# Performance work log

Measured on AMD Instinct MI355X. Metric: run time of the kernel, lower is better.

## Reference

```python
import jax, jax.numpy as jnp
import numpy as np

H = 1024
V = 32000
L = 15
B = 512


def setup_inputs() -> dict:
    key = jax.random.key(0)
    ks = jax.random.split(key, 16)
    s = 0.02
    return {
        "input_ids": jax.random.randint(ks[0], (B,), 0, V),
        "hidden": jax.random.normal(ks[1], (1, B, H), jnp.float32),
        "encoder_outputs": jax.random.normal(ks[2], (L, B, H), jnp.float32),
        "max_length": L,
        "embedding": jax.random.normal(ks[3], (V, H), jnp.float32) * s,
        "attn1_w": jax.random.normal(ks[4], (1, 2 * H), jnp.float32) * s,
        "attn1_b": jnp.zeros((1,), jnp.float32),
        "combine_w": jax.random.normal(ks[5], (H, 2 * H), jnp.float32) * s,
        "combine_b": jnp.zeros((H,), jnp.float32),
        "w_ih": jax.random.normal(ks[6], (3 * H, H), jnp.float32) * s,
        "w_hh": jax.random.normal(ks[7], (3 * H, H), jnp.float32) * s,
        "b_ih": jnp.zeros((3 * H,), jnp.float32),
        "b_hh": jnp.zeros((3 * H,), jnp.float32),
        "out_w": jax.random.normal(ks[8], (V, H), jnp.float32) * s,
        "out_b": jnp.zeros((V,), jnp.float32),
    }


def reference(input_ids, hidden, encoder_outputs, max_length, embedding,
              attn1_w, attn1_b, combine_w, combine_b,
              w_ih, w_hh, b_ih, b_hh, out_w, out_b):
    # embedding lookup (dropout is identity in eval mode)
    emb = embedding[input_ids]                       # [B, H]
    # Bahdanau-style additive scores: vectorize the per-step python loop
    emb_l = jnp.broadcast_to(emb[None], (max_length, B, H))   # [L, B, H]
    cat = jnp.concatenate([emb_l, encoder_outputs], axis=-1)  # [L, B, 2H]
    scores = cat @ attn1_w.T + attn1_b               # [L, B, 1]
    attn_weights = jax.nn.softmax(scores, axis=0)    # softmax over L
    ctx = jnp.sum(attn_weights * encoder_outputs, axis=0)     # [B, H]
    x = jnp.concatenate([emb, ctx], axis=-1) @ combine_w.T + combine_b  # [B, H]
    # n_layers = 1: relu then one GRU step (seq len 1)
    x = jax.nn.relu(x)
    h = hidden[0]                                    # [B, H]
    gi = x @ w_ih.T + b_ih                           # [B, 3H]
    gh = h @ w_hh.T + b_hh                           # [B, 3H]
    i_r, i_z, i_n = jnp.split(gi, 3, axis=1)
    h_r, h_z, h_n = jnp.split(gh, 3, axis=1)
    r = jax.nn.sigmoid(i_r + h_r)
    z = jax.nn.sigmoid(i_z + h_z)
    n = jnp.tanh(i_n + r * h_n)
    h_new = (1.0 - z) * n + z * h                    # [B, H]
    logits = h_new @ out_w.T + out_b                 # [B, V]
    output = jax.nn.log_softmax(logits, axis=1)
    return output, h_new[None], attn_weights
```

## Files before the change

### kernel.cpp

```cpp
#include <hip/hip_runtime.h>

#define HH 1024
#define VV 32000
#define LL 15
#define BB 512

typedef __bf16 bf16;
typedef __bf16 bf16x4 __attribute__((ext_vector_type(4)));
typedef __bf16 bf16x8 __attribute__((ext_vector_type(8)));
typedef float f32x4 __attribute__((ext_vector_type(4)));

#define VMCNT(n) asm volatile("s_waitcnt vmcnt(" #n ")" ::: "memory")
#define SBAR     __builtin_amdgcn_s_barrier()
#define SCHED0   __builtin_amdgcn_sched_barrier(0)

__device__ __forceinline__ unsigned short f2bf(float f) {
    unsigned int u = __float_as_uint(f);
    unsigned int r = (u + 0x7fffu + ((u >> 16) & 1u)) >> 16;
    return (unsigned short)r;
}

__device__ __forceinline__ void gld_lds16(const void* g, void* l) {
    __builtin_amdgcn_global_load_lds(
        (const __attribute__((address_space(1))) unsigned int*)g,
        (__attribute__((address_space(3))) unsigned int*)l, 16, 0, 0);
}

__global__ __launch_bounds__(256)
void cvt4_kernel(const float* __restrict__ a0, unsigned short* __restrict__ o0, int n0_,
                 const float* __restrict__ a1, unsigned short* __restrict__ o1, int n1_,
                 const float* __restrict__ a2, unsigned short* __restrict__ o2, int n2_,
                 const float* __restrict__ a3, unsigned short* __restrict__ o3, int n3_) {
    int i = blockIdx.x * 256 + threadIdx.x;
    const float* src; unsigned short* dst;
    if (i < n0_) { src = a0; dst = o0; }
    else if ((i -= n0_) < n1_) { src = a1; dst = o1; }
    else if ((i -= n1_) < n2_) { src = a2; dst = o2; }
    else if ((i -= n2_) < n3_) { src = a3; dst = o3; }
    else return;
    const f32x4 a = ((const f32x4*)src)[2 * i], b = ((const f32x4*)src)[2 * i + 1];
    ((bf16x4*)dst)[2 * i]     = __builtin_convertvector(a, bf16x4);
    ((bf16x4*)dst)[2 * i + 1] = __builtin_convertvector(b, bf16x4);
}

__global__ __launch_bounds__(256)
void pack_w(const float* __restrict__ src, unsigned short* __restrict__ dst) {
    const int b = blockIdx.x;
    const int g = b >> 2, q = b & 3;
    const float* pan = src + (size_t)g * 65536;
    char* pd = (char*)(dst + (size_t)g * 65536);
    #pragma unroll
    for (int j = 0; j < 16; j++) {
        const int s4 = q * 4096 + j * 256 + threadIdx.x;
        const f32x4 v = ((const f32x4*)pan)[s4];
        const int sp = s4 * 4;
        const int r = sp >> 10, k = sp & 1023;
        bf16x4 w = __builtin_convertvector(v, bf16x4);
        *(bf16x4*)(pd + ((k >> 6) << 13) + (r << 7) + ((k & 63) << 1)) = w;
    }
}

__global__ __launch_bounds__(256)
void attn_kernel(const int* __restrict__ ids, const float* __restrict__ enc,
                 const float* __restrict__ embedding,
                 const float* __restrict__ attn1_w, const float* __restrict__ attn1_b,
                 float* __restrict__ attn_out, unsigned short* __restrict__ cat_out) {
    const int b = blockIdx.x, tid = threadIdx.x;
    const int lane = tid & 63, wv = tid >> 6;

    __shared__ float s_enc[LL * HH];
    __shared__ float s_scores[LL];
    __shared__ float s_red[4];

    for (int idx = tid; idx < LL * HH / 4; idx += 256) {
        const int l = (idx * 4) >> 10, h = (idx * 4) & (HH - 1);
        *(f32x4*)&s_enc[idx * 4] = *(const f32x4*)&enc[((size_t)l * BB + b) * HH + h];
    }

    const float* embr = embedding + (size_t)ids[b] * HH;
    float p = 0.f;
    for (int j = tid; j < HH; j += 256) p += embr[j] * attn1_w[j];
    #pragma unroll
    for (int o = 32; o; o >>= 1) p += __shfl_xor(p, o);
    if (lane == 0) s_red[wv] = p;
    __syncthreads();
    const float semb = s_red[0] + s_red[1] + s_red[2] + s_red[3] + attn1_b[0];

    for (int l = wv; l < LL; l += 4) {
        float q = 0.f;
        for (int j = lane; j < HH; j += 64) q += s_enc[l * HH + j] * attn1_w[HH + j];
        #pragma unroll
        for (int o = 32; o; o >>= 1) q += __shfl_xor(q, o);
        if (lane == 0) s_scores[l] = q + semb;
    }
    __syncthreads();

    float mx = -3.4e38f;
    #pragma unroll
    for (int l = 0; l < LL; l++) mx = fmaxf(mx, s_scores[l]);
    float aw[LL], sum = 0.f;
    #pragma unroll
    for (int l = 0; l < LL; l++) { aw[l] = __expf(s_scores[l] - mx); sum += aw[l]; }
    const float inv = 1.f / sum;
    #pragma unroll
    for (int l = 0; l < LL; l++) aw[l] *= inv;

    if (tid < LL) attn_out[tid * BB + b] = aw[tid];

    for (int j = tid; j < HH; j += 256) {
        float c = 0.f;
        #pragma unroll
        for (int l = 0; l < LL; l++) c += aw[l] * s_enc[l * HH + j];
        cat_out[(size_t)b * (2 * HH) + j] = f2bf(embr[j]);
        cat_out[(size_t)b * (2 * HH) + HH + j] = f2bf(c);
    }
}

template<int TM, int TN, int OUT, int GATES>
__global__ __launch_bounds__(256)
void gemm_nt(const bf16* __restrict__ A, const bf16* __restrict__ B,
             const float* __restrict__ bias, void* __restrict__ Cout,
             const bf16* __restrict__ A2, const bf16* __restrict__ B2,
             const float* __restrict__ bias2, void* __restrict__ C2,
             const int K, const int N) {
    constexpr int FM = TM / 32, FN = TN / 32;
    __shared__ bf16 As[2][TM * 64];
    __shared__ bf16 Bs[2][TN * 64];

    if (GATES && blockIdx.z == 1) { A = A2; B = B2; bias = bias2; Cout = C2; }

    const int tid = threadIdx.x;
    const int lane = tid & 63, wave = tid >> 6;
    const int wm = wave >> 1, wn = wave & 1;
    const int rlo = lane & 15, khi = lane >> 4;
    const int m0 = blockIdx.y * TM, n0 = blockIdx.x * TN;

    f32x4 acc[FM][FN] = {};
    constexpr int IA = TM / 32, IB = TN / 32;

    auto stage = [&](int k0, int buf) {
        #pragma unroll
        for (int i = 0; i < IA; i++) {
            const int p = (i * 256 + tid) * 16;
            const int row = p >> 7;
            const int qs = (p & 127) ^ ((row & 7) << 4);
            gld_lds16(A + (size_t)(m0 + row) * K + k0 + (qs >> 1),
                      &As[buf][0] + i * 2048 + wave * 512);
        }
        #pragma unroll
        for (int i = 0; i < IB; i++) {
            const int p = (i * 256 + tid) * 16;
            const int row = p >> 7;
            const int qs = (p & 127) ^ ((row & 7) << 4);
            gld_lds16(B + (size_t)(n0 + row) * K + k0 + (qs >> 1),
                      &Bs[buf][0] + i * 2048 + wave * 512);
        }
    };

    auto compute = [&](int buf) {
        #pragma unroll
        for (int ks = 0; ks < 2; ks++) {
            bf16x8 af[FM], bfr[FN];
            #pragma unroll
            for (int m = 0; m < FM; m++) {
                const int r = wm * (TM / 2) + m * 16 + rlo;
                const int sw = (ks * 64 + khi * 16) ^ ((r & 7) << 4);
                af[m] = *(const bf16x8*)((const char*)&As[buf][0] + r * 128 + sw);
            }
            #pragma unroll
            for (int n = 0; n < FN; n++) {
                const int r = wn * (TN / 2) + n * 16 + rlo;
                const int sw = (ks * 64 + khi * 16) ^ ((r & 7) << 4);
                bfr[n] = *(const bf16x8*)((const char*)&Bs[buf][0] + r * 128 + sw);
            }
            #pragma unroll
            for (int m = 0; m < FM; m++)
                #pragma unroll
                for (int n = 0; n < FN; n++)
                    acc[m][n] = __builtin_amdgcn_mfma_f32_16x16x32_bf16(af[m], bfr[n], acc[m][n], 0, 0, 0);
        }
    };

    const int NT = K >> 6;
    stage(0, 0);
    stage(64, 1);

    for (int kt = 0; kt < NT; kt += 2) {
        {
            const int t = kt;
            if (t + 1 < NT) { VMCNT(4); } else { VMCNT(0); }
            SCHED0; SBAR; SCHED0;
            compute(0);
            SCHED0; SBAR; SCHED0;
            if (t + 2 < NT) stage((t + 2) << 6, 0);
        }
        {
            const int t = kt + 1;
            if (t + 1 < NT) { VMCNT(4); } else { VMCNT(0); }
            SCHED0; SBAR; SCHED0;
            compute(1);
            SCHED0; SBAR; SCHED0;
            if (t + 2 < NT) stage((t + 2) << 6, 1);
        }
    }

    #pragma unroll
    for (int m = 0; m < FM; m++) {
        const int gr = m0 + wm * (TM / 2) + m * 16 + khi * 4;
        #pragma unroll
        for (int n = 0; n < FN; n++) {
            const int gc = n0 + wn * (TN / 2) + n * 16 + rlo;
            const float bv = bias[gc];
            #pragma unroll
            for (int j = 0; j < 4; j++) {
                float v = acc[m][n][j] + bv;
                if (OUT == 1) {
                    v = fmaxf(v, 0.f);
                    ((unsigned short*)Cout)[(size_t)(gr + j) * N + gc] = f2bf(v);
                } else {
                    ((float*)Cout)[(size_t)(gr + j) * N + gc] = v;
                }
            }
        }
    }
}

__global__ __launch_bounds__(256, 3)
void gemm_out(const bf16* __restrict__ A, const bf16* __restrict__ Bp,
              const float* __restrict__ bias, float* __restrict__ C,
              float* __restrict__ pmax, float* __restrict__ psum, const int nbase) {
    constexpr int K = HH, N = VV;
    __shared__ bf16 As[2][128 * 64];
    __shared__ bf16 Bs[2][64 * 64];
    __shared__ float sPm[2][128], sPs[2][128];

    const int tid = threadIdx.x;
    const int lane = tid & 63, wave = tid >> 6;
    const int wm = wave >> 1, wn = wave & 1;
    const int rlo = lane & 15, khi = lane >> 4;

    constexpr int gridN = 250;
    constexpr int nFull = (gridN >> 3) << 5;
    const int bidx = blockIdx.x;
    int g, jm;
    if (bidx < nFull) { const int s = bidx >> 5, rem = bidx & 31; jm = rem >> 3; g = s * 8 + (rem & 7); }
    else { const int rem = bidx - nFull; constexpr int gleft = gridN & 7; g = (gridN & ~7) + rem % gleft; jm = rem / gleft; }
    const int n0 = nbase + g * 64, m0 = jm * 128;

    const char* tile_base = (const char*)Bp + (size_t)g * 131072;

    f32x4 acc[4][2] = {};

    auto stage = [&](int k0, int buf) {
        #pragma unroll
        for (int i = 0; i < 4; i++) {
            const int p = (i * 256 + tid) * 16;
            const int row = p >> 7;
            const int qs = (p & 127) ^ ((row & 7) << 4);
            gld_lds16(A + (size_t)(m0 + row) * K + k0 + (qs >> 1),
                      &As[buf][0] + i * 2048 + wave * 512);
        }
        #pragma unroll
        for (int i = 0; i < 2; i++) {
            const int p = (i * 256 + tid) * 16;
            const int row = p >> 7;
            const int qs = (p & 127) ^ ((row & 7) << 4);
            gld_lds16(tile_base + (size_t)k0 * 128 + row * 128 + qs,
                      &Bs[buf][0] + i * 2048 + wave * 512);
        }
    };

    auto compute = [&](int buf) {
        #pragma unroll
        for (int ks = 0; ks < 2; ks++) {
            bf16x8 af[4], bfr[2];
            #pragma unroll
            for (int m = 0; m < 4; m++) {
                const int r = wm * 64 + m * 16 + rlo;
                const int sw = (ks * 64 + khi * 16) ^ ((r & 7) << 4);
                af[m] = *(const bf16x8*)((const char*)&As[buf][0] + r * 128 + sw);
            }
            #pragma unroll
            for (int n = 0; n < 2; n++) {
                const int r = wn * 32 + n * 16 + rlo;
                const int sw = (ks * 64 + khi * 16) ^ ((r & 7) << 4);
                bfr[n] = *(const bf16x8*)((const char*)&Bs[buf][0] + r * 128 + sw);
            }
            #pragma unroll
            for (int m = 0; m < 4; m++)
                #pragma unroll
                for (int n = 0; n < 2; n++)
                    acc[m][n] = __builtin_amdgcn_mfma_f32_16x16x32_bf16(af[m], bfr[n], acc[m][n], 0, 0, 0);
        }
    };

    constexpr int NT = K >> 6;
    stage(0, 0);
    stage(64, 1);

    for (int kt = 0; kt < NT; kt += 2) {
        {
            const int t = kt;
            if (t + 1 < NT) { VMCNT(6); } else { VMCNT(0); }
            SCHED0; SBAR; SCHED0;
            compute(0);
            SCHED0; SBAR; SCHED0;
            if (t + 2 < NT) stage((t + 2) << 6, 0);
        }
        {
            const int t = kt + 1;
            if (t + 1 < NT) { VMCNT(6); } else { VMCNT(0); }
            SCHED0; SBAR; SCHED0;
            compute(1);
            SCHED0; SBAR; SCHED0;
            if (t + 2 < NT) stage((t + 2) << 6, 1);
        }
    }

    float bvn[2];
    #pragma unroll
    for (int n = 0; n < 2; n++) bvn[n] = bias[n0 + wn * 32 + n * 16 + rlo];

    #pragma unroll
    for (int m = 0; m < 4; m++) {
        const int rbase = wm * 64 + m * 16 + khi * 4;
        #pragma unroll
        for (int j = 0; j < 4; j++) {
            const int gr = m0 + rbase + j;
            float v[2];
            #pragma unroll
            for (int n = 0; n < 2; n++) {
                v[n] = acc[m][n][j] + bvn[n];
                C[(size_t)gr * N + n0 + wn * 32 + n * 16 + rlo] = v[n];
            }
            float lm = fmaxf(v[0], v[1]);
            #pragma unroll
            for (int o = 8; o; o >>= 1) lm = fmaxf(lm, __shfl_xor(lm, o));
            float ls = __expf(v[0] - lm) + __expf(v[1] - lm);
            #pragma unroll
            for (int o = 8; o; o >>= 1) ls += __shfl_xor(ls, o);
            if (rlo == 0) { sPm[wn][rbase + j] = lm; sPs[wn][rbase + j] = ls; }
        }
    }
    __syncthreads();
    if (tid < 128) {
        const float ma = sPm[0][tid], mb = sPm[1][tid];
        const float M = fmaxf(ma, mb);
        const float S = sPs[0][tid] * __expf(ma - M) + sPs[1][tid] * __expf(mb - M);
        const int gg = (nbase >> 6) + g;
        pmax[(size_t)(m0 + tid) * 512 + gg] = M;
        psum[(size_t)(m0 + tid) * 512 + gg] = S;
    }
}

__global__ __launch_bounds__(256)
void gru_kernel(const float* __restrict__ gi, const float* __restrict__ gh,
                const float* __restrict__ h, float* __restrict__ hnew,
                unsigned short* __restrict__ hnew_bf) {
    const int i = blockIdx.x * 256 + threadIdx.x;
    const int e = i * 4;
    const int b = e >> 10, j = e & (HH - 1);
    const size_t o = ((size_t)b * 3 * HH + j) / 4;
    const f32x4 ir = ((const f32x4*)gi)[o],          iz = ((const f32x4*)gi)[o + HH / 4],
                in_ = ((const f32x4*)gi)[o + 2 * HH / 4];
    const f32x4 hr = ((const f32x4*)gh)[o],          hz = ((const f32x4*)gh)[o + HH / 4],
                hn = ((const f32x4*)gh)[o + 2 * HH / 4];
    const f32x4 hv = ((const f32x4*)h)[i];
    f32x4 out;
    ushort4 ob;
    #pragma unroll
    for (int c = 0; c < 4; c++) {
        const float r = 1.f / (1.f + __expf(-(ir[c] + hr[c])));
        const float z = 1.f / (1.f + __expf(-(iz[c] + hz[c])));
        const float n = tanhf(in_[c] + r * hn[c]);
        const float v = (1.f - z) * n + z * hv[c];
        out[c] = v;
        ((unsigned short*)&ob)[c] = f2bf(v);
    }
    ((f32x4*)hnew)[i] = out;
    ((ushort4*)hnew_bf)[i] = ob;
}

__global__ __launch_bounds__(512)
void lsm_final(const float* __restrict__ pmax, const float* __restrict__ psum,
               float* __restrict__ logits) {
    const int b = blockIdx.x, tid = threadIdx.x;
    const int lane = tid & 63, wv = tid >> 6;
    __shared__ float sm[8], ss[8];

    float m = -3.4e38f, s = 0.f;
    if (tid < VV / 64) { m = pmax[(size_t)b * 512 + tid]; s = psum[(size_t)b * 512 + tid]; }
    #pragma unroll
    for (int o = 32; o; o >>= 1) {
        const float mo = __shfl_xor(m, o), so = __shfl_xor(s, o);
        const float nm = fmaxf(m, mo);
        s = s * __expf(m - nm) + so * __expf(mo - nm);
        m = nm;
    }
    if (lane == 0) { sm[wv] = m; ss[wv] = s; }
    __syncthreads();
    float M = sm[0], S;
    #pragma unroll
    for (int w = 1; w < 8; w++) M = fmaxf(M, sm[w]);
    S = ss[0] * __expf(sm[0] - M);
    #pragma unroll
    for (int w = 1; w < 8; w++) S += ss[w] * __expf(sm[w] - M);
    const float lse = M + __logf(S);

    float* row = logits + (size_t)b * VV;
    for (int j = tid; j < VV / 4; j += 512) {
        f32x4 v = ((const f32x4*)row)[j];
        v[0] -= lse; v[1] -= lse; v[2] -= lse; v[3] -= lse;
        ((f32x4*)row)[j] = v;
    }
}

extern "C" void kernel_launch(void* const* d_in, const int* in_sizes, int n_in,
                              void* d_out, int out_size, void* d_ws, size_t ws_size,
                              hipStream_t stream) {
    const int*   ids       = (const int*)d_in[0];
    const float* hidden    = (const float*)d_in[1];
    const float* enc       = (const float*)d_in[2];
    const float* embedding = (const float*)d_in[4];
    const float* attn1_w   = (const float*)d_in[5];
    const float* attn1_b   = (const float*)d_in[6];
    const float* combine_w = (const float*)d_in[7];
    const float* combine_b = (const float*)d_in[8];
    const float* w_ih      = (const float*)d_in[9];
    const float* w_hh      = (const float*)d_in[10];
    const float* b_ih      = (const float*)d_in[11];
    const float* b_hh      = (const float*)d_in[12];
    const float* out_w     = (const float*)d_in[13];
    const float* out_b     = (const float*)d_in[14];

    float* out_lsm = (float*)d_out;
    float* out_h   = out_lsm + (size_t)BB * VV;
    float* out_aw  = out_h + (size_t)BB * HH;

    char* w = (char*)d_ws;
    unsigned short* w_ih_bf  = (unsigned short*)w;   w += (size_t)3 * HH * HH * 2;
    unsigned short* w_hh_bf  = (unsigned short*)w;   w += (size_t)3 * HH * HH * 2;
    unsigned short* w_cb_bf  = (unsigned short*)w;   w += (size_t)2 * HH * HH * 2;
    unsigned short* cat_bf   = (unsigned short*)w;   w += (size_t)BB * 2 * HH * 2;
    unsigned short* x_bf     = (unsigned short*)w;   w += (size_t)BB * HH * 2;
    unsigned short* hid_bf   = (unsigned short*)w;   w += (size_t)BB * HH * 2;
    unsigned short* hnew_bf  = (unsigned short*)w;   w += (size_t)BB * HH * 2;
    float* gi   = (float*)w;                         w += (size_t)BB * 3 * HH * 4;
    float* gh   = (float*)w;                         w += (size_t)BB * 3 * HH * 4;
    float* pmax = (float*)w;                         w += (size_t)BB * 512 * 4;
    float* psum = (float*)w;                         w += (size_t)BB * 512 * 4;
    unsigned short* packed = (unsigned short*)w;     w += (size_t)16000 * HH * 2;

    cvt4_kernel<<<(3 * HH * HH / 8 * 2 + 2 * HH * HH / 8 + BB * HH / 8) / 256, 256, 0, stream>>>(
        w_ih, w_ih_bf, 3 * HH * HH / 8,
        w_hh, w_hh_bf, 3 * HH * HH / 8,
        combine_w, w_cb_bf, 2 * HH * HH / 8,
        hidden, hid_bf, BB * HH / 8);

    attn_kernel<<<BB, 256, 0, stream>>>(ids, enc, embedding, attn1_w, attn1_b, out_aw, cat_bf);

    gemm_nt<64, 64, 1, 0><<<dim3(HH / 64, BB / 64), 256, 0, stream>>>(
        (const bf16*)cat_bf, (const bf16*)w_cb_bf, combine_b, x_bf,
        nullptr, nullptr, nullptr, nullptr, 2 * HH, HH);

    gemm_nt<64, 64, 0, 1><<<dim3(3 * HH / 64, BB / 64, 2), 256, 0, stream>>>(
        (const bf16*)hid_bf, (const bf16*)w_hh_bf, b_hh, gh,
        (const bf16*)x_bf, (const bf16*)w_ih_bf, b_ih, gi, HH, 3 * HH);

    gru_kernel<<<(BB * HH / 4) / 256, 256, 0, stream>>>(gi, gh, hidden, out_h, hnew_bf);

    pack_w<<<1000, 256, 0, stream>>>(out_w, packed);
    gemm_out<<<1000, 256, 0, stream>>>(
        (const bf16*)hnew_bf, (const bf16*)packed, out_b, out_lsm, pmax, psum, 0);

    pack_w<<<1000, 256, 0, stream>>>(out_w + (size_t)16000 * HH, packed);
    gemm_out<<<1000, 256, 0, stream>>>(
        (const bf16*)hnew_bf, (const bf16*)packed, out_b, out_lsm, pmax, psum, 16000);

    lsm_final<<<BB, 512, 0, stream>>>(pmax, psum, out_lsm);
}
```

Baseline: 208.6 us.

## Pack full output weight once and widen vocab GEMM tile to 128 columns

The output projection weight is now packed to bf16 in one pass into a full-size workspace buffer before the other kernels. This replaces two half-size pack/GEMM pairs with one GEMM launch. The GEMM tile grows from 128x64 to 128x128, so each wave holds a 4x4 MFMA accumulator block and A-tile reuse doubles. Occupancy is lowered from 3 to 2 blocks per CU, and the partial softmax buffers shrink to 250 column groups per row. The cost is more LDS and registers per block and a larger workspace.

```diff
diff --git a/kernel.cpp b/kernel.cpp
--- a/kernel.cpp
+++ b/kernel.cpp
@@ -24,6 +24,24 @@
     __builtin_amdgcn_global_load_lds(
         (const __attribute__((address_space(1))) unsigned int*)g,
         (__attribute__((address_space(3))) unsigned int*)l, 16, 0, 0);
+}
+
+__global__ __launch_bounds__(256)
+void pack_w(const float* __restrict__ src, unsigned short* __restrict__ dst) {
+    const int bid = blockIdx.x;
+    const int g = bid >> 3, rq = bid & 7;
+    const float* s0 = src + ((size_t)g * 128 + rq * 16) * 1024;
+    unsigned short* d0 = dst + (size_t)g * (16 * 128 * 64);
+    #pragma unroll
+    for (int j = 0; j < 16; j++) {
+        const int s4 = j * 256 + threadIdx.x;
+        const f32x4 v = ((const f32x4*)s0)[s4];
+        const int sp = s4 * 4;
+        const int rl = rq * 16 + (sp >> 10);
+        const int k = sp & 1023;
+        bf16x4 w = __builtin_convertvector(v, bf16x4);
+        *(bf16x4*)&d0[(size_t)(k >> 6) * 8192 + rl * 64 + (k & 63)] = w;
+    }
 }
 
 __global__ __launch_bounds__(256)
@@ -44,23 +62,6 @@
 }
 
 __global__ __launch_bounds__(256)
-void pack_w(const float* __restrict__ src, unsigned short* __restrict__ dst) {
-    const int b = blockIdx.x;
-    const int g = b >> 2, q = b & 3;
-    const float* pan = src + (size_t)g * 65536;
-    char* pd = (char*)(dst + (size_t)g * 65536);
-    #pragma unroll
-    for (int j = 0; j < 16; j++) {
-        const int s4 = q * 4096 + j * 256 + threadIdx.x;
-        const f32x4 v = ((const f32x4*)pan)[s4];
-        const int sp = s4 * 4;
-        const int r = sp >> 10, k = sp & 1023;
-        bf16x4 w = __builtin_convertvector(v, bf16x4);
-        *(bf16x4*)(pd + ((k >> 6) << 13) + (r << 7) + ((k & 63) << 1)) = w;
-    }
-}
-
-__global__ __launch_bounds__(256)
 void attn_kernel(const int* __restrict__ ids, const float* __restrict__ enc,
                  const float* __restrict__ embedding,
                  const float* __restrict__ attn1_w, const float* __restrict__ attn1_b,
@@ -225,13 +226,13 @@
     }
 }
 
-__global__ __launch_bounds__(256, 3)
+__global__ __launch_bounds__(256, 2)
 void gemm_out(const bf16* __restrict__ A, const bf16* __restrict__ Bp,
               const float* __restrict__ bias, float* __restrict__ C,
-              float* __restrict__ pmax, float* __restrict__ psum, const int nbase) {
+              float* __restrict__ pmax, float* __restrict__ psum) {
     constexpr int K = HH, N = VV;
     __shared__ bf16 As[2][128 * 64];
-    __shared__ bf16 Bs[2][64 * 64];
+    __shared__ bf16 Bs[2][128 * 64];
     __shared__ float sPm[2][128], sPs[2][128];
 
     const int tid = threadIdx.x;
@@ -245,11 +246,11 @@
     int g, jm;
     if (bidx < nFull) { const int s = bidx >> 5, rem = bidx & 31; jm = rem >> 3; g = s * 8 + (rem & 7); }
     else { const int rem = bidx - nFull; constexpr int gleft = gridN & 7; g = (gridN & ~7) + rem % gleft; jm = rem / gleft; }
-    const int n0 = nbase + g * 64, m0 = jm * 128;
-
-    const char* tile_base = (const char*)Bp + (size_t)g * 131072;
-
-    f32x4 acc[4][2] = {};
+    const int n0 = g * 128, m0 = jm * 128;
+
+    const char* pb = (const char*)(Bp + (size_t)g * 131072);
+
+    f32x4 acc[4][4] = {};
 
     auto stage = [&](int k0, int buf) {
         #pragma unroll
@@ -261,11 +262,11 @@
                       &As[buf][0] + i * 2048 + wave * 512);
         }
         #pragma unroll
-        for (int i = 0; i < 2; i++) {
+        for (int i = 0; i < 4; i++) {
             const int p = (i * 256 + tid) * 16;
             const int row = p >> 7;
             const int qs = (p & 127) ^ ((row & 7) << 4);
-            gld_lds16(tile_base + (size_t)k0 * 128 + row * 128 + qs,
+            gld_lds16(pb + (size_t)(k0 >> 6) * 16384 + row * 128 + qs,
                       &Bs[buf][0] + i * 2048 + wave * 512);
         }
     };
@@ -273,7 +274,7 @@
     auto compute = [&](int buf) {
         #pragma unroll
         for (int ks = 0; ks < 2; ks++) {
-            bf16x8 af[4], bfr[2];
+            bf16x8 af[4], bfr[4];
             #pragma unroll
             for (int m = 0; m < 4; m++) {
                 const int r = wm * 64 + m * 16 + rlo;
@@ -281,15 +282,15 @@
                 af[m] = *(const bf16x8*)((const char*)&As[buf][0] + r * 128 + sw);
             }
             #pragma unroll
-            for (int n = 0; n < 2; n++) {
-                const int r = wn * 32 + n * 16 + rlo;
+            for (int n = 0; n < 4; n++) {
+                const int r = wn * 64 + n * 16 + rlo;
                 const int sw = (ks * 64 + khi * 16) ^ ((r & 7) << 4);
                 bfr[n] = *(const bf16x8*)((const char*)&Bs[buf][0] + r * 128 + sw);
             }
             #pragma unroll
             for (int m = 0; m < 4; m++)
                 #pragma unroll
-                for (int n = 0; n < 2; n++)
+                for (int n = 0; n < 4; n++)
                     acc[m][n] = __builtin_amdgcn_mfma_f32_16x16x32_bf16(af[m], bfr[n], acc[m][n], 0, 0, 0);
         }
     };
@@ -301,7 +302,7 @@
     for (int kt = 0; kt < NT; kt += 2) {
         {
             const int t = kt;
-            if (t + 1 < NT) { VMCNT(6); } else { VMCNT(0); }
+            if (t + 1 < NT) { VMCNT(8); } else { VMCNT(0); }
             SCHED0; SBAR; SCHED0;
             compute(0);
             SCHED0; SBAR; SCHED0;
@@ -309,7 +310,7 @@
         }
         {
             const int t = kt + 1;
-            if (t + 1 < NT) { VMCNT(6); } else { VMCNT(0); }
+            if (t + 1 < NT) { VMCNT(8); } else { VMCNT(0); }
             SCHED0; SBAR; SCHED0;
             compute(1);
             SCHED0; SBAR; SCHED0;
@@ -317,9 +318,9 @@
         }
     }
 
-    float bvn[2];
-    #pragma unroll
-    for (int n = 0; n < 2; n++) bvn[n] = bias[n0 + wn * 32 + n * 16 + rlo];
+    float bvn[4];
+    #pragma unroll
+    for (int n = 0; n < 4; n++) bvn[n] = bias[n0 + wn * 64 + n * 16 + rlo];
 
     #pragma unroll
     for (int m = 0; m < 4; m++) {
@@ -327,16 +328,19 @@
         #pragma unroll
         for (int j = 0; j < 4; j++) {
             const int gr = m0 + rbase + j;
-            float v[2];
-            #pragma unroll
-            for (int n = 0; n < 2; n++) {
+            float v[4];
+            float lm = -3.4e38f;
+            #pragma unroll
+            for (int n = 0; n < 4; n++) {
                 v[n] = acc[m][n][j] + bvn[n];
-                C[(size_t)gr * N + n0 + wn * 32 + n * 16 + rlo] = v[n];
-            }
-            float lm = fmaxf(v[0], v[1]);
+                C[(size_t)gr * N + n0 + wn * 64 + n * 16 + rlo] = v[n];
+                lm = fmaxf(lm, v[n]);
+            }
             #pragma unroll
             for (int o = 8; o; o >>= 1) lm = fmaxf(lm, __shfl_xor(lm, o));
-            float ls = __expf(v[0] - lm) + __expf(v[1] - lm);
+            float ls = 0.f;
+            #pragma unroll
+            for (int n = 0; n < 4; n++) ls += __expf(v[n] - lm);
             #pragma unroll
             for (int o = 8; o; o >>= 1) ls += __shfl_xor(ls, o);
             if (rlo == 0) { sPm[wn][rbase + j] = lm; sPs[wn][rbase + j] = ls; }
@@ -347,9 +351,8 @@
         const float ma = sPm[0][tid], mb = sPm[1][tid];
         const float M = fmaxf(ma, mb);
         const float S = sPs[0][tid] * __expf(ma - M) + sPs[1][tid] * __expf(mb - M);
-        const int gg = (nbase >> 6) + g;
-        pmax[(size_t)(m0 + tid) * 512 + gg] = M;
-        psum[(size_t)(m0 + tid) * 512 + gg] = S;
+        pmax[(size_t)(m0 + tid) * 256 + g] = M;
+        psum[(size_t)(m0 + tid) * 256 + g] = S;
     }
 }
 
@@ -389,7 +392,7 @@
     __shared__ float sm[8], ss[8];
 
     float m = -3.4e38f, s = 0.f;
-    if (tid < VV / 64) { m = pmax[(size_t)b * 512 + tid]; s = psum[(size_t)b * 512 + tid]; }
+    if (tid < 250) { m = pmax[(size_t)b * 256 + tid]; s = psum[(size_t)b * 256 + tid]; }
     #pragma unroll
     for (int o = 32; o; o >>= 1) {
         const float mo = __shfl_xor(m, o), so = __shfl_xor(s, o);
@@ -438,6 +441,7 @@
     float* out_aw  = out_h + (size_t)BB * HH;
 
     char* w = (char*)d_ws;
+    unsigned short* packed   = (unsigned short*)w;   w += (size_t)VV * HH * 2;
     unsigned short* w_ih_bf  = (unsigned short*)w;   w += (size_t)3 * HH * HH * 2;
     unsigned short* w_hh_bf  = (unsigned short*)w;   w += (size_t)3 * HH * HH * 2;
     unsigned short* w_cb_bf  = (unsigned short*)w;   w += (size_t)2 * HH * HH * 2;
@@ -447,10 +451,10 @@
     unsigned short* hnew_bf  = (unsigned short*)w;   w += (size_t)BB * HH * 2;
     float* gi   = (float*)w;                         w += (size_t)BB * 3 * HH * 4;
     float* gh   = (float*)w;                         w += (size_t)BB * 3 * HH * 4;
-    float* pmax = (float*)w;                         w += (size_t)BB * 512 * 4;
-    float* psum = (float*)w;                         w += (size_t)BB * 512 * 4;
-    unsigned short* packed = (unsigned short*)w;     w += (size_t)16000 * HH * 2;
-
+    float* pmax = (float*)w;                         w += (size_t)BB * 256 * 4;
+    float* psum = (float*)w;                         w += (size_t)BB * 256 * 4;
+
+    pack_w<<<2000, 256, 0, stream>>>(out_w, packed);
     cvt4_kernel<<<(3 * HH * HH / 8 * 2 + 2 * HH * HH / 8 + BB * HH / 8) / 256, 256, 0, stream>>>(
         w_ih, w_ih_bf, 3 * HH * HH / 8,
         w_hh, w_hh_bf, 3 * HH * HH / 8,
@@ -469,13 +473,8 @@
 
     gru_kernel<<<(BB * HH / 4) / 256, 256, 0, stream>>>(gi, gh, hidden, out_h, hnew_bf);
 
-    pack_w<<<1000, 256, 0, stream>>>(out_w, packed);
     gemm_out<<<1000, 256, 0, stream>>>(
-        (const bf16*)hnew_bf, (const bf16*)packed, out_b, out_lsm, pmax, psum, 0);
-
-    pack_w<<<1000, 256, 0, stream>>>(out_w + (size_t)16000 * HH, packed);
-    gemm_out<<<1000, 256, 0, stream>>>(
-        (const bf16*)hnew_bf, (const bf16*)packed, out_b, out_lsm, pmax, psum, 16000);
+        (const bf16*)hnew_bf, (const bf16*)packed, out_b, out_lsm, pmax, psum);
 
     lsm_final<<<BB, 512, 0, stream>>>(pmax, psum, out_lsm);
 }
```

Measured after the change: 182.2 us. -12.7%, faster.
